# Optimization experiments

Measured on AMD Instinct MI355X. Metric: run time of the kernel, lower is better.

## Reference

```python
import jax, jax.numpy as jnp
import numpy as np

B, N, G = 1, 8192, 512      # batch, n_cells, n_genes
D_DEN = 512                  # denoise hidden
D_EMB1, D_EMB = 256, 32      # embed hidden / final embed dim
D_Q = 64                     # quality hidden
H = 4                        # interaction heads
LBD = 1.0


def _lin_init(key, fan_in, fan_out):
    # torch nn.Linear default init (uniform +/- 1/sqrt(fan_in)); stored as [in,out]
    k1, k2 = jax.random.split(key)
    bound = 1.0 / np.sqrt(fan_in)
    W = jax.random.uniform(k1, (fan_in, fan_out), minval=-bound, maxval=bound, dtype=jnp.float32)
    b = jax.random.uniform(k2, (fan_out,), minval=-bound, maxval=bound, dtype=jnp.float32)
    return W, b


def setup_inputs() -> dict:
    key = jax.random.key(0)
    ks = jax.random.split(key, 9)
    raw_expr = jax.random.normal(ks[0], (B, N, G), dtype=jnp.float32)
    dW1, db1 = _lin_init(ks[1], G, D_DEN)
    dW2, db2 = _lin_init(ks[2], D_DEN, G)
    eW1, eb1 = _lin_init(ks[3], G, D_EMB1)
    eW2, eb2 = _lin_init(ks[4], D_EMB1, D_EMB)
    qW1, qb1 = _lin_init(ks[5], G, D_Q)
    qW2, qb2 = _lin_init(ks[6], D_Q, 1)
    # CellInteract.transform: xavier_normal -> std = sqrt(2/(d+d)) = 1/sqrt(d)
    transforms = jax.random.normal(ks[7], (H, D_EMB, D_EMB), dtype=jnp.float32) * np.float32(1.0 / np.sqrt(D_EMB))
    # gene_response is a trained parameter (zeros at init); random so path is non-trivial
    gene_responses = jax.random.normal(ks[8], (H, G, G), dtype=jnp.float32) * np.float32(0.02)
    return dict(raw_expr=raw_expr, dW1=dW1, db1=db1, dW2=dW2, db2=db2,
                eW1=eW1, eb1=eb1, eW2=eW2, eb2=eb2,
                qW1=qW1, qb1=qb1, qW2=qW2, qb2=qb2,
                transforms=transforms, gene_responses=gene_responses)


def _cdist(x):
    # pairwise euclidean distance over cells: [B,N,D] -> [B,N,N], grad-safe at 0
    sq = jnp.sum(x * x, axis=-1)
    d2 = sq[..., :, None] + sq[..., None, :] - 2.0 * jnp.einsum('bnd,bmd->bnm', x, x)
    d2 = jnp.maximum(d2, 0.0)
    eps = 1e-12
    safe = jnp.where(d2 > eps, d2, eps)
    return jnp.where(d2 > eps, jnp.sqrt(safe), 0.0)


def reference(raw_expr, dW1, db1, dW2, db2, eW1, eb1, eW2, eb2,
              qW1, qb1, qW2, qb2, transforms, gene_responses):
    # CellDenoise: Linear-Tanh-Linear + residual
    denoised = jnp.tanh(raw_expr @ dW1 + db1) @ dW2 + db2 + raw_expr      # [B,N,G]
    # CellQualify: Linear-Tanh-Linear -> [B,N,1]
    quality = jnp.tanh(raw_expr @ qW1 + qb1) @ qW2 + qb2
    # CellEmbed: Linear-Tanh-Linear -> [B,N,D_EMB]
    enc = jnp.tanh(raw_expr @ eW1 + eb1) @ eW2 + eb2
    # CellSmooth: softmax(-cdist + quality^T) @ denoised
    scores = -_cdist(enc) + jnp.swapaxes(quality, -1, -2)                 # [B,N,N]
    sim = jax.nn.softmax(scores, axis=-1)
    smoothed = sim @ denoised                                             # [B,N,G]
    # CellInteract heads (interact=True path): sigmoid(enc T enc^T) @ expr @ gene_response / N
    inter = jnp.zeros_like(smoothed)
    for h in range(H):
        ci = jax.nn.sigmoid(jnp.einsum('bnd,de,bme->bnm', enc, transforms[h], enc))
        inter = inter + (ci @ smoothed) @ gene_responses[h] / N
    final = smoothed + LBD * inter
    return denoised, smoothed, final
```

## Files before the change

kernel.cpp:

```cpp
#include <hip/hip_runtime.h>
#include <hip/hip_bf16.h>
#include <stdint.h>
#if !__has_builtin(__builtin_amdgcn_cvt_pk_fp8_f32)
#include <hip/hip_fp8.h>
#endif

#define NC 8192
#define GG 512

typedef __attribute__((ext_vector_type(8))) short bf16x8;
typedef __attribute__((ext_vector_type(4))) float fx4;
typedef __attribute__((ext_vector_type(4))) unsigned int uint4v;
typedef __attribute__((ext_vector_type(2))) long long llx2;

__device__ __forceinline__ float bf2f(short s){
  union { uint32_t u; float f; } c; c.u = ((uint32_t)(uint16_t)s) << 16; return c.f;
}
__device__ __forceinline__ short f2bf(float f){
  union { float f; uint32_t u; } c; c.f = f;
  uint32_t u = c.u;
  uint32_t r = (u + 0x7fffu + ((u >> 16) & 1u)) >> 16;
  return (short)(uint16_t)r;
}
__device__ __forceinline__ uint32_t au(float f){
  union { float f; uint32_t u; } c; c.f = f; return c.u;
}
#if __has_builtin(__builtin_amdgcn_rcpf)
__device__ __forceinline__ float fast_rcp(float x){ return __builtin_amdgcn_rcpf(x); }
#else
__device__ __forceinline__ float fast_rcp(float x){ return 1.0f / x; }
#endif
#if __has_builtin(__builtin_amdgcn_sqrtf)
__device__ __forceinline__ float fast_sqrt(float x){ return __builtin_amdgcn_sqrtf(x); }
#else
__device__ __forceinline__ float fast_sqrt(float x){ return sqrtf(x); }
#endif
__device__ __forceinline__ float tanh_fast(float x){
  float e = __expf(2.0f * x);
  return 1.0f - 2.0f * fast_rcp(e + 1.0f);
}
__device__ __forceinline__ uint32_t pack_bf(float lo, float hi){
  return __builtin_amdgcn_perm(au(hi) + 0x8000u, au(lo) + 0x8000u, 0x07060302u);
}
template<bool HI>
__device__ __forceinline__ uint32_t pk_fp8(float a, float b, uint32_t old){
#if __has_builtin(__builtin_amdgcn_cvt_pk_fp8_f32)
  return (uint32_t)__builtin_amdgcn_cvt_pk_fp8_f32(a, b, (int)old, HI);
#else
  __hip_fp8_e4m3 fa(a), fb(b);
  uint32_t v = (uint32_t)fa.__x | ((uint32_t)fb.__x << 8);
  return HI ? ((old & 0x0000ffffu) | (v << 16)) : ((old & 0xffff0000u) | v);
#endif
}
__device__ __forceinline__ void g2l16(const void* g, void* l){
  __builtin_amdgcn_global_load_lds((const __attribute__((address_space(1))) void*)g,
                                   (__attribute__((address_space(3))) void*)l, 16, 0, 0);
}

__global__ void cast_f32_bf16(const float* __restrict__ in, short* __restrict__ out, int n){
  int i = (blockIdx.x * 256 + threadIdx.x) * 4;
  if (i < n){
    float4 v = *(const float4*)(in + i);
    uint32_t lo = (uint32_t)(uint16_t)f2bf(v.x) | ((uint32_t)(uint16_t)f2bf(v.y) << 16);
    uint32_t hi = (uint32_t)(uint16_t)f2bf(v.z) | ((uint32_t)(uint16_t)f2bf(v.w) << 16);
    *(uint2*)(out + i) = make_uint2(lo, hi);
  }
}

__global__ void transpose_cast(const float* __restrict__ in, short* __restrict__ out,
                               int R, int C, int ostride, int roff, int permute){
  __shared__ float t[32][33];
  int c0 = blockIdx.x * 32, r0 = blockIdx.y * 32;
  int x = threadIdx.x & 31, y = threadIdx.x >> 5;
  #pragma unroll
  for (int it = 0; it < 4; ++it)
    t[y + 8*it][x] = in[(size_t)(r0 + y + 8*it) * C + c0 + x];
  __syncthreads();
  int xp = permute ? (((x >> 2) & 3) * 8 + ((x >> 4) & 1) * 4 + (x & 3)) : x;
  #pragma unroll
  for (int it = 0; it < 4; ++it)
    out[(size_t)(c0 + y + 8*it) * ostride + roff + r0 + xp] = f2bf(t[x][y + 8*it]);
}

__global__ void transpose_cast8(const float* __restrict__ in, unsigned char* __restrict__ out,
                                int C, int ostride){
  __shared__ float t[32][33];
  int c0 = blockIdx.x * 32, r0 = blockIdx.y * 32;
  int x = threadIdx.x & 31, y = threadIdx.x >> 5;
  #pragma unroll
  for (int it = 0; it < 4; ++it)
    t[y + 8*it][x] = in[(size_t)(r0 + y + 8*it) * C + c0 + x];
  __syncthreads();
  int xp = ((x >> 2) & 3) * 16 + ((r0 >> 5) & 1) * 8 + ((x >> 4) & 1) * 4 + (x & 3);
  int cb = r0 & ~63;
  #pragma unroll
  for (int it = 0; it < 4; ++it){
    float v = t[x][y + 8*it];
    out[(size_t)(c0 + y + 8*it) * ostride + cb + xp] =
        (unsigned char)(pk_fp8<false>(v, v, 0u) & 0xffu);
  }
}

__global__ void fill_bias(const float* __restrict__ db1, const float* __restrict__ eb1,
                          const float* __restrict__ qb1, float* __restrict__ b){
  int i = blockIdx.x * 256 + threadIdx.x;
  if (i >= 896) return;
  float v = 0.0f;
  if (i < 512) v = db1[i];
  else if (i < 768) v = eb1[i - 512];
  else if (i < 832) v = qb1[i - 768];
  b[i] = v;
}

__global__ __launch_bounds__(256, 2)
void gemm_bt(const short* __restrict__ A, int lda, const short* __restrict__ B, int ldb,
             int K, int mode, const float* __restrict__ bias,
             const float* __restrict__ res, int ldres,
             float* __restrict__ outf, short* __restrict__ outb, int ldo, float scale)
{
  __shared__ __align__(16) short As[64 * 64];
  __shared__ __align__(16) short Bs[128 * 64];
  const int tid = threadIdx.x;
  const int lane = tid & 63, wave = tid >> 6;
  const int wm = wave >> 1, wn = wave & 1;
  const int l16 = lane & 15, q = lane >> 4;
  const size_t i0 = (size_t)blockIdx.y * 64;
  const int n0 = blockIdx.x * 128;
  fx4 acc[2][4] = {};

  for (int k0 = 0; k0 < K; k0 += 64){
    #pragma unroll
    for (int inst = 0; inst < 2; ++inst){
      int ch = inst * 256 + tid;
      int r = ch >> 3, pc = ch & 7;
      int colc = (pc ^ (r & 7)) * 8;
      g2l16(A + (i0 + r) * (size_t)lda + k0 + colc, As + ch * 8);
    }
    #pragma unroll
    for (int inst = 0; inst < 4; ++inst){
      int ch = inst * 256 + tid;
      int r = ch >> 3, pc = ch & 7;
      int colc = (pc ^ (r & 7)) * 8;
      g2l16(B + (size_t)(n0 + r) * (size_t)ldb + k0 + colc, Bs + ch * 8);
    }
    __syncthreads();
    #pragma unroll
    for (int ks = 0; ks < 2; ++ks){
      int k8 = ks * 4 + q;
      bf16x8 af[2], bfr[4];
      #pragma unroll
      for (int mi = 0; mi < 2; ++mi){
        int r = wm * 32 + mi * 16 + l16;
        af[mi] = *(const bf16x8*)(As + r * 64 + ((k8 ^ (r & 7)) << 3));
      }
      #pragma unroll
      for (int ni = 0; ni < 4; ++ni){
        int r = wn * 64 + ni * 16 + l16;
        bfr[ni] = *(const bf16x8*)(Bs + r * 64 + ((k8 ^ (r & 7)) << 3));
      }
      #pragma unroll
      for (int mi = 0; mi < 2; ++mi)
        #pragma unroll
        for (int ni = 0; ni < 4; ++ni)
          acc[mi][ni] = __builtin_amdgcn_mfma_f32_16x16x32_bf16(af[mi], bfr[ni], acc[mi][ni], 0, 0, 0);
    }
    __syncthreads();
  }
  #pragma unroll
  for (int mi = 0; mi < 2; ++mi){
    #pragma unroll
    for (int ni = 0; ni < 4; ++ni){
      int n = n0 + wn * 64 + ni * 16 + l16;
      float b = bias ? bias[n] : 0.0f;
      #pragma unroll
      for (int r = 0; r < 4; ++r){
        size_t m = i0 + wm * 32 + mi * 16 + q * 4 + r;
        float v = acc[mi][ni][r];
        size_t o = m * (size_t)ldo + n;
        if (mode == 0)      outb[o] = f2bf(tanh_fast(v + b));
        else if (mode == 1) outf[o] = v + b + res[m * (size_t)ldres + n];
        else                outf[o] += v * scale;
      }
    }
  }
}

template<int GT, int CH, int MODE, int ISL>
__global__ __launch_bounds__(256, (MODE == 0) ? 4 : 2)
void attn_reg(const short* __restrict__ encA, const short* __restrict__ encJ,
              const short* __restrict__ VTp,
              const float* __restrict__ sq, const float* __restrict__ E,
              float* __restrict__ out0, float* __restrict__ out1,
              short* __restrict__ outb, int ldo)
{
  constexpr int NG  = GT / 16;
  constexpr int KS  = CH / 32;
  constexpr int CPR = CH / 8;
  constexpr int SH  = (CPR == 4) ? 1 : 0;
  constexpr int HB  = GT * CH;
  __shared__ __align__(16) short Vl[2 * HB];
  const int tid = threadIdx.x, lane = tid & 63, wave = tid >> 6;
  const int l16 = lane & 15, q = lane >> 4;
  const int ib = blockIdx.y * (64 * ISL) + wave * 16;
  const int g0 = blockIdx.x * GT;
  const short* Ai = encA + (size_t)blockIdx.z * NC * 32;

  bf16x8 bi[ISL];
  float sqi[ISL], lacc[ISL];
  #pragma unroll
  for (int s = 0; s < ISL; ++s){
    bi[s] = *(const bf16x8*)(Ai + (size_t)(ib + s * 64 + l16) * 32 + q * 8);
    lacc[s] = 0.f;
    sqi[s] = (MODE == 0) ? sq[ib + s * 64 + l16] : 0.f;
  }
  fx4 acc[ISL][NG] = {};
  uint4v bP[ISL][KS], bPn[ISL][KS];

  auto stage = [&](int jc, int buf){
    #pragma unroll
    for (int inst = 0; inst < HB / 2048; ++inst){
      int ch = inst * 256 + tid;
      int r = ch / CPR, pc = ch % CPR;
      int colc = (pc ^ ((r >> SH) & (CPR - 1))) * 8;
      g2l16(VTp + (size_t)(g0 + r) * NC + jc + colc, Vl + buf * HB + ch * 8);
    }
  };
  auto transform = [&](int jb, uint4v (*o)[KS]){
    #pragma unroll
    for (int ks = 0; ks < KS; ++ks){
      uint32_t dw[ISL][4];
      #pragma unroll
      for (int jt = 0; jt < 2; ++jt){
        int j0t = jb + ks * 32 + jt * 16;
        bf16x8 aj = *(const bf16x8*)(encJ + (size_t)(j0t + l16) * 32 + q * 8);
        float4 sqj = {}, Ej = {};
        if (MODE == 0){
          sqj = *(const float4*)(sq + j0t + q * 4);
          Ej  = *(const float4*)(E  + j0t + q * 4);
        }
        #pragma unroll
        for (int s = 0; s < ISL; ++s){
          fx4 c = {};
          c = __builtin_amdgcn_mfma_f32_16x16x32_bf16(aj, bi[s], c, 0, 0, 0);
          float pv[4];
          #pragma unroll
          for (int r = 0; r < 4; ++r){
            float dot = c[r];
            if (MODE == 0){
              float d2 = fmaxf(sqi[s] + ((const float*)&sqj)[r] - 2.0f * dot, 0.0f);
              float p = ((const float*)&Ej)[r] * __expf(-fast_sqrt(d2));
              lacc[s] += p;
              pv[r] = p;
            } else {
              pv[r] = fast_rcp(1.0f + __expf(-dot));
            }
          }
          dw[s][jt * 2]     = pack_bf(pv[0], pv[1]);
          dw[s][jt * 2 + 1] = pack_bf(pv[2], pv[3]);
        }
      }
      #pragma unroll
      for (int s = 0; s < ISL; ++s){
        uint4v u = { dw[s][0], dw[s][1], dw[s][2], dw[s][3] };
        o[s][ks] = u;
      }
    }
  };
  auto pv_step = [&](int buf){
    #pragma unroll
    for (int ks = 0; ks < KS; ++ks){
      int k8 = ks * 4 + q;
      #pragma unroll
      for (int gt = 0; gt < NG; ++gt){
        int rr = gt * 16 + l16;
        bf16x8 av = *(const bf16x8*)(Vl + buf * HB + rr * CH +
                                     ((k8 ^ ((rr >> SH) & (CPR - 1))) << 3));
        #pragma unroll
        for (int s = 0; s < ISL; ++s)
          acc[s][gt] = __builtin_amdgcn_mfma_f32_16x16x32_bf16(
              av, *(const bf16x8*)&bP[s][ks], acc[s][gt], 0, 0, 0);
      }
    }
  };

  stage(0, 0);
  transform(0, bP);
  __syncthreads();
  for (int jc = 0; jc < NC; jc += CH){
    int buf = (jc / CH) & 1;
    int nxt = jc + CH;
    if (nxt < NC){
      stage(nxt, buf ^ 1);
      transform(nxt, bPn);
    }
    pv_step(buf);
    #pragma unroll
    for (int s = 0; s < ISL; ++s)
      #pragma unroll
      for (int ks = 0; ks < KS; ++ks) bP[s][ks] = bPn[s][ks];
    if (nxt < NC) __syncthreads();
  }

  #pragma unroll
  for (int s = 0; s < ISL; ++s){
    int irow = ib + s * 64 + l16;
    if (MODE == 0){
      float v = lacc[s];
      v += __shfl_xor(v, 16);
      v += __shfl_xor(v, 32);
      float inv = fast_rcp(v);
      #pragma unroll
      for (int gt = 0; gt < NG; ++gt){
        int g = g0 + gt * 16 + q * 4;
        float4 o;
        o.x = acc[s][gt][0] * inv; o.y = acc[s][gt][1] * inv;
        o.z = acc[s][gt][2] * inv; o.w = acc[s][gt][3] * inv;
        size_t off = (size_t)irow * GG + g;
        *(float4*)(out0 + off) = o;
        *(float4*)(out1 + off) = o;
      }
    } else {
      #pragma unroll
      for (int gt = 0; gt < NG; ++gt){
        int g = g0 + gt * 16 + q * 4;
        uint2 u;
        u.x = pack_bf(acc[s][gt][0], acc[s][gt][1]);
        u.y = pack_bf(acc[s][gt][2], acc[s][gt][3]);
        *(uint2*)(outb + (size_t)irow * ldo + (size_t)blockIdx.z * GG + g) = u;
      }
    }
  }
}

__global__ __launch_bounds__(256, 2)
void attn_f8(const short* __restrict__ encA, const short* __restrict__ encJ,
             const unsigned char* __restrict__ V8, short* __restrict__ outb, int ldo)
{
  __shared__ __align__(16) unsigned char Vl[2 * 512 * 64];
  const int tid = threadIdx.x, lane = tid & 63, wave = tid >> 6;
  const int l16 = lane & 15, q = lane >> 4;
  const int i0 = blockIdx.y * 64 + wave * 16;
  const short* Ai = encA + (size_t)blockIdx.z * NC * 32;
  const bf16x8 bi = *(const bf16x8*)(Ai + (size_t)(i0 + l16) * 32 + q * 8);
  fx4 acc[32] = {};
  uint2 bP[2], bPn[2];

  auto stage = [&](int jc, int buf){
    #pragma unroll
    for (int inst = 0; inst < 8; ++inst){
      int ch = inst * 256 + tid;
      int r = ch >> 2, pc = ch & 3;
      int colc = (pc ^ ((r >> 1) & 3)) * 16;
      g2l16(V8 + (size_t)r * NC + jc + colc, Vl + buf * 32768 + ch * 16);
    }
  };
  auto transform = [&](int jb, uint2* o){
    #pragma unroll
    for (int ks = 0; ks < 2; ++ks){
      uint32_t dw[2];
      #pragma unroll
      for (int jt = 0; jt < 2; ++jt){
        int j0t = jb + ks * 32 + jt * 16;
        bf16x8 aj = *(const bf16x8*)(encJ + (size_t)(j0t + l16) * 32 + q * 8);
        fx4 c = {};
        c = __builtin_amdgcn_mfma_f32_16x16x32_bf16(aj, bi, c, 0, 0, 0);
        float p[4];
        #pragma unroll
        for (int r = 0; r < 4; ++r)
          p[r] = fast_rcp(1.0f + __expf(-c[r]));
        dw[jt] = pk_fp8<true>(p[2], p[3], pk_fp8<false>(p[0], p[1], 0u));
      }
      o[ks] = make_uint2(dw[0], dw[1]);
    }
  };
  auto pv_step = [&](int buf){
    const long long bp0 = *(const long long*)&bP[0];
    const long long bp1 = *(const long long*)&bP[1];
    #pragma unroll
    for (int gt = 0; gt < 32; ++gt){
      int rr = gt * 16 + l16;
      llx2 av = *(const llx2*)(Vl + buf * 32768 + rr * 64 + ((q ^ ((rr >> 1) & 3)) << 4));
      acc[gt] = __builtin_amdgcn_mfma_f32_16x16x32_fp8_fp8(av[0], bp0, acc[gt], 0, 0, 0);
      acc[gt] = __builtin_amdgcn_mfma_f32_16x16x32_fp8_fp8(av[1], bp1, acc[gt], 0, 0, 0);
    }
  };

  stage(0, 0);
  transform(0, bP);
  __syncthreads();
  for (int jc = 0; jc < NC; jc += 64){
    int buf = (jc >> 6) & 1;
    int nxt = jc + 64;
    if (nxt < NC){
      stage(nxt, buf ^ 1);
      transform(nxt, bPn);
    }
    pv_step(buf);
    bP[0] = bPn[0]; bP[1] = bPn[1];
    if (nxt < NC) __syncthreads();
  }

  #pragma unroll
  for (int gt = 0; gt < 32; ++gt){
    int g = gt * 16 + q * 4;
    uint2 u;
    u.x = pack_bf(acc[gt][0], acc[gt][1]);
    u.y = pack_bf(acc[gt][2], acc[gt][3]);
    *(uint2*)(outb + (size_t)(i0 + l16) * ldo + (size_t)blockIdx.z * GG + g) = u;
  }
}

__global__ void embed2_kernel(const short* __restrict__ H2, int lda,
                              const float* __restrict__ eW2,
                              const float* __restrict__ eb2, const float* __restrict__ T4,
                              short* __restrict__ encb, float* __restrict__ sq,
                              short* __restrict__ Ah)
{
  __shared__ float encS[8][32];
  int d = threadIdx.x & 31, cl = threadIdx.x >> 5;
  size_t c = (size_t)blockIdx.x * 8 + cl;
  float s = eb2[d];
  const short* hrow = H2 + c * lda;
  for (int k = 0; k < 256; ++k) s += bf2f(hrow[k]) * eW2[k * 32 + d];
  short eb = f2bf(s);
  encb[c * 32 + d] = eb;
  encS[cl][d] = bf2f(eb);
  __syncthreads();
  if (d == 0){
    float t = 0;
    for (int k = 0; k < 32; ++k) t += encS[cl][k] * encS[cl][k];
    sq[c] = t;
  }
  #pragma unroll
  for (int h = 0; h < 4; ++h){
    float a = 0;
    const float* T = T4 + h * 1024;
    for (int k = 0; k < 32; ++k) a += encS[cl][k] * T[k * 32 + d];
    Ah[(size_t)h * NC * 32 + c * 32 + d] = f2bf(a);
  }
}

__global__ void qtail_kernel(const short* __restrict__ Hq, int lda,
                             const float* __restrict__ qW2, const float* __restrict__ qb2,
                             float* __restrict__ E)
{
  int j = threadIdx.x & 63, cl = threadIdx.x >> 6;
  size_t c = (size_t)blockIdx.x * 4 + cl;
  float t = bf2f(Hq[c * lda + j]) * qW2[j];
  #pragma unroll
  for (int o = 32; o >= 1; o >>= 1) t += __shfl_xor(t, o);
  if (j == 0) E[c] = __expf(t + qb2[0]);
}

extern "C" void kernel_launch(void* const* d_in, const int* in_sizes, int n_in,
                              void* d_out, int out_size, void* d_ws, size_t ws_size,
                              hipStream_t stream)
{
  const float* raw = (const float*)d_in[0];
  const float* dW1 = (const float*)d_in[1];
  const float* db1 = (const float*)d_in[2];
  const float* dW2 = (const float*)d_in[3];
  const float* db2 = (const float*)d_in[4];
  const float* eW1 = (const float*)d_in[5];
  const float* eb1 = (const float*)d_in[6];
  const float* eW2 = (const float*)d_in[7];
  const float* eb2 = (const float*)d_in[8];
  const float* qW1 = (const float*)d_in[9];
  const float* qb1 = (const float*)d_in[10];
  const float* qW2 = (const float*)d_in[11];
  const float* qb2 = (const float*)d_in[12];
  const float* Tr  = (const float*)d_in[13];
  const float* Gr  = (const float*)d_in[14];

  float* outD = (float*)d_out;
  float* outS = outD + (size_t)NC * GG;
  float* outF = outS + (size_t)NC * GG;

  char* ws = (char*)d_ws;
  size_t off = 0;
  auto take = [&](size_t bytes) -> char* {
    char* p = ws + off; off += (bytes + 255) & ~(size_t)255; return p;
  };
  short* Xb    = (short*)take((size_t)NC * GG * 2);
  short* WcatT = (short*)take((size_t)896 * 512 * 2);
  short* dW2T  = (short*)take((size_t)512 * 512 * 2);
  short* GTc   = (short*)take((size_t)512 * 2048 * 2);
  float* bcat  = (float*)take((size_t)896 * 4);
  short* Hcat  = (short*)take((size_t)NC * 896 * 2);
  short* denTp = (short*)take((size_t)GG * NC * 2);
  unsigned char* smoT8 = (unsigned char*)take((size_t)GG * NC);
  short* encb  = (short*)take((size_t)NC * 32 * 2);
  short* Ahb   = (short*)take((size_t)4 * NC * 32 * 2);
  float* sqv   = (float*)take((size_t)NC * 4);
  float* Ev    = (float*)take((size_t)NC * 4);
  short* Ucat  = (short*)take((size_t)NC * 2048 * 2);

  dim3 b256(256);
  cast_f32_bf16<<<dim3((NC * GG) / 1024), b256, 0, stream>>>(raw, Xb, NC * GG);
  transpose_cast<<<dim3(16, 16), b256, 0, stream>>>(dW1, WcatT, 512, 512, 512, 0, 0);
  transpose_cast<<<dim3(8, 16),  b256, 0, stream>>>(eW1, WcatT + 512 * 512, 512, 256, 512, 0, 0);
  transpose_cast<<<dim3(2, 16),  b256, 0, stream>>>(qW1, WcatT + 768 * 512, 512, 64, 512, 0, 0);
  transpose_cast<<<dim3(16, 16), b256, 0, stream>>>(dW2, dW2T, 512, 512, 512, 0, 0);
  for (int h = 0; h < 4; ++h)
    transpose_cast<<<dim3(16, 16), b256, 0, stream>>>(Gr + (size_t)h * 512 * 512,
                                                      GTc, 512, 512, 2048, h * 512, 0);
  fill_bias<<<dim3(4), b256, 0, stream>>>(db1, eb1, qb1, bcat);
  gemm_bt<<<dim3(7, 128), b256, 0, stream>>>(Xb, 512, WcatT, 512, 512, 0, bcat,
                                             (const float*)nullptr, 0,
                                             (float*)nullptr, Hcat, 896, 1.0f);
  gemm_bt<<<dim3(4, 128), b256, 0, stream>>>(Hcat, 896, dW2T, 512, 512, 1, db2,
                                             raw, 512, outD, (short*)nullptr, 512, 1.0f);
  transpose_cast<<<dim3(16, 256), b256, 0, stream>>>(outD, denTp, NC, 512, NC, 0, 1);
  embed2_kernel<<<dim3(NC / 8), b256, 0, stream>>>(Hcat + 512, 896, eW2, eb2, Tr,
                                                   encb, sqv, Ahb);
  qtail_kernel<<<dim3(NC / 4), b256, 0, stream>>>(Hcat + 768, 896, qW2, qb2, Ev);
  attn_reg<128, 64, 0, 1><<<dim3(4, 128, 1), b256, 0, stream>>>(
      encb, encb, denTp, sqv, Ev, outS, outF, (short*)nullptr, 0);
  transpose_cast8<<<dim3(16, 256), b256, 0, stream>>>(outS, smoT8, 512, NC);
  attn_f8<<<dim3(1, 128, 4), b256, 0, stream>>>(Ahb, encb, smoT8, Ucat, 2048);
  gemm_bt<<<dim3(4, 128), b256, 0, stream>>>(Ucat, 2048, GTc, 2048, 2048,
                                             3, (const float*)nullptr,
                                             (const float*)nullptr, 0,
                                             outF, (short*)nullptr, 512, 1.0f / NC);
}
```

Measured before the change: 750.0 us.

## Share sigmoid probability tiles via LDS and split gene columns across waves

In the fp8 attention-like kernel, each wave used to compute P for its own 16 rows and then multiply it against all 512 gene columns of V. Now each wave writes its fp8 P fragment into a double-buffered LDS tile. In pv_step every wave reads all four row tiles and handles only its 128-column slice of V. Each V fragment loaded from LDS is now reused across 4 row tiles instead of 1, cutting V LDS reads per MFMA, in exchange for extra P writes and reads through LDS. The number of accumulators stays the same.

```diff
diff --git a/kernel.cpp b/kernel.cpp
--- a/kernel.cpp
+++ b/kernel.cpp
@@ -337,13 +337,13 @@
              const unsigned char* __restrict__ V8, short* __restrict__ outb, int ldo)
 {
   __shared__ __align__(16) unsigned char Vl[2 * 512 * 64];
+  __shared__ __align__(16) unsigned char Pl[2 * 4096];
   const int tid = threadIdx.x, lane = tid & 63, wave = tid >> 6;
   const int l16 = lane & 15, q = lane >> 4;
-  const int i0 = blockIdx.y * 64 + wave * 16;
+  const int i0 = blockIdx.y * 64;
   const short* Ai = encA + (size_t)blockIdx.z * NC * 32;
-  const bf16x8 bi = *(const bf16x8*)(Ai + (size_t)(i0 + l16) * 32 + q * 8);
-  fx4 acc[32] = {};
-  uint2 bP[2], bPn[2];
+  const bf16x8 bi = *(const bf16x8*)(Ai + (size_t)(i0 + wave * 16 + l16) * 32 + q * 8);
+  fx4 acc[4][8] = {};
 
   auto stage = [&](int jc, int buf){
     #pragma unroll
@@ -354,10 +354,10 @@
       g2l16(V8 + (size_t)r * NC + jc + colc, Vl + buf * 32768 + ch * 16);
     }
   };
-  auto transform = [&](int jb, uint2* o){
+  auto transform = [&](int jb, int buf){
+    uint32_t dwa[2][2];
     #pragma unroll
     for (int ks = 0; ks < 2; ++ks){
-      uint32_t dw[2];
       #pragma unroll
       for (int jt = 0; jt < 2; ++jt){
         int j0t = jb + ks * 32 + jt * 16;
@@ -368,45 +368,54 @@
         #pragma unroll
         for (int r = 0; r < 4; ++r)
           p[r] = fast_rcp(1.0f + __expf(-c[r]));
-        dw[jt] = pk_fp8<true>(p[2], p[3], pk_fp8<false>(p[0], p[1], 0u));
-      }
-      o[ks] = make_uint2(dw[0], dw[1]);
-    }
+        dwa[ks][jt] = pk_fp8<true>(p[2], p[3], pk_fp8<false>(p[0], p[1], 0u));
+      }
+    }
+    uint4v u = { dwa[0][0], dwa[0][1], dwa[1][0], dwa[1][1] };
+    *(uint4v*)(Pl + buf * 4096 + ((wave * 4 + q) * 16 + l16) * 16) = u;
   };
   auto pv_step = [&](int buf){
-    const long long bp0 = *(const long long*)&bP[0];
-    const long long bp1 = *(const long long*)&bP[1];
-    #pragma unroll
-    for (int gt = 0; gt < 32; ++gt){
-      int rr = gt * 16 + l16;
+    llx2 pf[4];
+    #pragma unroll
+    for (int it = 0; it < 4; ++it)
+      pf[it] = *(const llx2*)(Pl + buf * 4096 + ((it * 4 + q) * 16 + l16) * 16);
+    #pragma unroll
+    for (int gt = 0; gt < 8; ++gt){
+      int rr = wave * 128 + gt * 16 + l16;
       llx2 av = *(const llx2*)(Vl + buf * 32768 + rr * 64 + ((q ^ ((rr >> 1) & 3)) << 4));
-      acc[gt] = __builtin_amdgcn_mfma_f32_16x16x32_fp8_fp8(av[0], bp0, acc[gt], 0, 0, 0);
-      acc[gt] = __builtin_amdgcn_mfma_f32_16x16x32_fp8_fp8(av[1], bp1, acc[gt], 0, 0, 0);
+      #pragma unroll
+      for (int it = 0; it < 4; ++it){
+        acc[it][gt] = __builtin_amdgcn_mfma_f32_16x16x32_fp8_fp8(av[0], pf[it][0], acc[it][gt], 0, 0, 0);
+        acc[it][gt] = __builtin_amdgcn_mfma_f32_16x16x32_fp8_fp8(av[1], pf[it][1], acc[it][gt], 0, 0, 0);
+      }
     }
   };
 
   stage(0, 0);
-  transform(0, bP);
+  transform(0, 0);
   __syncthreads();
   for (int jc = 0; jc < NC; jc += 64){
     int buf = (jc >> 6) & 1;
     int nxt = jc + 64;
     if (nxt < NC){
       stage(nxt, buf ^ 1);
-      transform(nxt, bPn);
+      transform(nxt, buf ^ 1);
     }
     pv_step(buf);
-    bP[0] = bPn[0]; bP[1] = bPn[1];
     if (nxt < NC) __syncthreads();
   }
 
   #pragma unroll
-  for (int gt = 0; gt < 32; ++gt){
-    int g = gt * 16 + q * 4;
-    uint2 u;
-    u.x = pack_bf(acc[gt][0], acc[gt][1]);
-    u.y = pack_bf(acc[gt][2], acc[gt][3]);
-    *(uint2*)(outb + (size_t)(i0 + l16) * ldo + (size_t)blockIdx.z * GG + g) = u;
+  for (int it = 0; it < 4; ++it){
+    int irow = i0 + it * 16 + l16;
+    #pragma unroll
+    for (int gt = 0; gt < 8; ++gt){
+      int g = wave * 128 + gt * 16 + q * 4;
+      uint2 u;
+      u.x = pack_bf(acc[it][gt][0], acc[it][gt][1]);
+      u.y = pack_bf(acc[it][gt][2], acc[it][gt][3]);
+      *(uint2*)(outb + (size_t)irow * ldo + (size_t)blockIdx.z * GG + g) = u;
+    }
   }
 }
 
```

Result: faster. 720.8 us (-3.9%).
